# Performance work log

Hardware: AMD Instinct MI355X
Metric: run time of the kernel (lower is better)

Reference implementation:

```python
import jax, jax.numpy as jnp
import numpy as np

NUM_HEADS = 16
TEMPERATURE = 1.0


def setup_inputs() -> dict:
    key = jax.random.key(0)
    ks = jax.random.split(key, 6)
    B, H = 2048, 2048
    return {
        "hidden_states": jax.random.normal(ks[0], (B, H), dtype=jnp.float32),
        "attention_mask": jnp.ones((B,), dtype=bool),
        "Wq": jax.random.normal(ks[1], (H, H), dtype=jnp.float32) * 0.02,
        "Wk": jax.random.normal(ks[2], (H, H), dtype=jnp.float32) * 0.02,
        "Wv": jax.random.normal(ks[3], (H, H), dtype=jnp.float32) * 0.02,
        "Wo": jax.random.normal(ks[4], (H, H), dtype=jnp.float32) * 0.02,
        "scale_param": jnp.full((1,), -3.0, dtype=jnp.float32),
    }


def reference(hidden_states, attention_mask, Wq, Wk, Wv, Wo, scale_param):
    B, H = hidden_states.shape
    nh = NUM_HEADS
    hd = H // nh
    # projections (torch Linear: x @ W.T), reshape to [heads, batch, head_dim]
    q = (hidden_states @ Wq.T).reshape(B, nh, hd).transpose(1, 0, 2)
    k = (hidden_states @ Wk.T).reshape(B, nh, hd).transpose(1, 0, 2)
    v = (hidden_states @ Wv.T).reshape(B, nh, hd).transpose(1, 0, 2)
    # cross-batch scores [heads, B, B]
    scores = jnp.einsum('hqd,hkd->hqk', q, k) / (hd ** 0.5 * TEMPERATURE)
    neg_inf = jnp.float32(-jnp.inf)
    eye = jnp.eye(B, dtype=bool)  # exclude self-attention (diagonal)
    scores = jnp.where(eye[None, :, :], neg_inf, scores)
    scores = jnp.where(attention_mask[None, None, :], scores, neg_inf)
    attn = jax.nn.softmax(scores, axis=-1)
    attn = jnp.nan_to_num(attn, nan=0.0)  # rows fully masked -> 0 (dropout=0 is identity)
    ctx = jnp.einsum('hqk,hkd->hqd', attn, v)  # [heads, B, head_dim]
    ctx = ctx.transpose(1, 0, 2).reshape(B, H)
    cross = ctx @ Wo.T
    scale = jax.nn.sigmoid(scale_param[0])
    return hidden_states + scale * cross
```

## Files before the change

kernel.cpp:

```cpp
#include <hip/hip_runtime.h>

typedef __bf16 bf16;
typedef __attribute__((ext_vector_type(8))) __bf16 bf16x8;
typedef __attribute__((ext_vector_type(4))) float f32x4;
typedef __attribute__((ext_vector_type(4))) short s16x4;

#define HDIM 2048

__device__ __forceinline__ void glds16(const void* g, void* l) {
  __builtin_amdgcn_global_load_lds((const __attribute__((address_space(1))) void*)g,
                                   (__attribute__((address_space(3))) void*)l,
                                   16, 0, 0);
}

#define MFMA16(a, b, c) __builtin_amdgcn_mfma_f32_16x16x32_bf16(a, b, c, 0, 0, 0)

__global__ __launch_bounds__(256) void cvt5(
    const float* __restrict__ s0, const float* __restrict__ s1,
    const float* __restrict__ s2, const float* __restrict__ s3,
    const float* __restrict__ s4,
    bf16* __restrict__ d0, bf16* __restrict__ d1, bf16* __restrict__ d2,
    bf16* __restrict__ d3, bf16* __restrict__ d4) {
  const float* s; bf16* d;
  switch (blockIdx.y) {
    case 0: s = s0; d = d0; break;
    case 1: s = s1; d = d1; break;
    case 2: s = s2; d = d2; break;
    case 3: s = s3; d = d3; break;
    default: s = s4; d = d4; break;
  }
  const size_t base = (size_t)blockIdx.x * 4096 + (threadIdx.x << 2);
  for (int i = 0; i < 4; i++) {
    const float4 v = *(const float4*)(s + base + i * 1024);
    union { bf16 h[4]; s16x4 s4v; } u;
    u.h[0] = (bf16)v.x; u.h[1] = (bf16)v.y; u.h[2] = (bf16)v.z; u.h[3] = (bf16)v.w;
    *(s16x4*)(d + base + i * 1024) = u.s4v;
  }
}

__device__ __forceinline__ void gemm128_core(const bf16* __restrict__ A,
                                             const bf16* __restrict__ B,
                                             int rowBase, int colBase,
                                             f32x4 acc[4][4],
                                             bf16* ldsA, bf16* ldsB) {
  const int t = threadIdx.x;
  const int w = t >> 6, l = t & 63;
  const int wr = (w >> 1) << 6, wc = (w & 1) << 6;
  const int lr = l & 15, lq = l >> 4;

  for (int mi = 0; mi < 4; mi++)
    for (int ni = 0; ni < 4; ni++)
      for (int r = 0; r < 4; r++) acc[mi][ni][r] = 0.f;

  const int sRow = (w << 4) + (l >> 2);
  const int sCol = (l & 3) << 3;
  const bf16* gA = A + (size_t)(rowBase + sRow) * HDIM + sCol;
  const bf16* gB = B + (size_t)(colBase + sRow) * HDIM + sCol;
  bf16* lA = ldsA + (w << 9);
  bf16* lB = ldsB + (w << 9);

  for (int k0 = 0; k0 < HDIM; k0 += 32) {
    glds16(gA, lA);
    glds16(gA + (size_t)64 * HDIM, lA + 2048);
    glds16(gB, lB);
    glds16(gB + (size_t)64 * HDIM, lB + 2048);
    gA += 32; gB += 32;
    __syncthreads();

    bf16x8 af[4], bfr[4];
    for (int mi = 0; mi < 4; mi++)
      af[mi] = *(const bf16x8*)&ldsA[(wr + mi * 16 + lr) * 32 + lq * 8];
    for (int ni = 0; ni < 4; ni++)
      bfr[ni] = *(const bf16x8*)&ldsB[(wc + ni * 16 + lr) * 32 + lq * 8];
    for (int mi = 0; mi < 4; mi++)
      for (int ni = 0; ni < 4; ni++)
        acc[mi][ni] = MFMA16(af[mi], bfr[ni], acc[mi][ni]);
    __syncthreads();
  }
}

__global__ __launch_bounds__(256) void qkv_gemm(
    const bf16* __restrict__ hs, const bf16* __restrict__ Wq,
    const bf16* __restrict__ Wk, const bf16* __restrict__ Wv,
    bf16* __restrict__ qb, bf16* __restrict__ Kf, bf16* __restrict__ Vf) {
  __shared__ bf16 ldsA[128 * 32];
  __shared__ bf16 ldsB[128 * 32];
  const int z = blockIdx.z;
  const bf16* W = (z == 0) ? Wq : (z == 1) ? Wk : Wv;
  const int rowBase = blockIdx.y << 7, colBase = blockIdx.x << 7;
  f32x4 acc[4][4];
  gemm128_core(hs, W, rowBase, colBase, acc, ldsA, ldsB);

  const int t = threadIdx.x;
  const int w = t >> 6, l = t & 63;
  const int wr = (w >> 1) << 6, wc = (w & 1) << 6;
  const int lr = l & 15, lq = l >> 4;

  if (z == 0) {
    for (int mi = 0; mi < 4; mi++)
      for (int ni = 0; ni < 4; ni++) {
        const int col = colBase + wc + ni * 16 + lr;
        const int row0 = rowBase + wr + mi * 16 + lq * 4;
        for (int r = 0; r < 4; r++)
          qb[(size_t)(row0 + r) * HDIM + col] = (bf16)acc[mi][ni][r];
      }
  } else if (z == 1) {
    for (int mi = 0; mi < 4; mi++)
      for (int ni = 0; ni < 4; ni++) {
        const int dim = colBase + wc + ni * 16 + lr;
        const int hh = dim >> 7, ks = (dim >> 5) & 3, kh = (dim >> 3) & 3, j = dim & 7;
        const int row0 = rowBase + wr + mi * 16 + lq * 4;
        for (int r = 0; r < 4; r++) {
          const int key = row0 + r;
          const int kbk = key >> 7, kni = (key >> 4) & 7, kl = key & 15;
          Kf[(((size_t)hh * 16 + kbk) * 32 + kni * 4 + ks) * 512 +
             (kh * 16 + kl) * 8 + j] = (bf16)acc[mi][ni][r];
        }
      }
  } else {
    for (int mi = 0; mi < 4; mi++)
      for (int ni = 0; ni < 4; ni++) {
        const int dim = colBase + wc + ni * 16 + lr;
        const int hh = dim >> 7, vni = (dim >> 4) & 7, ll = dim & 15;
        const int row0 = rowBase + wr + mi * 16 + lq * 4;
        const int kbk = row0 >> 7, ks = (row0 >> 5) & 3, lh = (row0 >> 3) & 3;
        const int j0 = row0 & 7;
        union { bf16 h4[4]; s16x4 v; } u;
        for (int r = 0; r < 4; r++) u.h4[r] = (bf16)acc[mi][ni][r];
        *(s16x4*)&Vf[(((size_t)hh * 16 + kbk) * 32 + vni * 4 + ks) * 512 +
                     (lh * 16 + ll) * 8 + j0] = u.v;
      }
  }
}

__global__ __launch_bounds__(256, 2) void attn_kernel(
    const bf16* __restrict__ qb, const bf16* __restrict__ Kf,
    const bf16* __restrict__ Vf, const unsigned char* __restrict__ amask,
    bf16* __restrict__ ctx) {
  __shared__ bf16 Kl[32 * 512];
  __shared__ bf16 Vl[32 * 512];
  __shared__ bf16 Pl[4 * 16 * 128];

  const int qt = blockIdx.x, h = blockIdx.y;
  const int t = threadIdx.x, w = t >> 6, l = t & 63;
  const int lr = l & 15, lq = l >> 4;
  bf16* Pw = Pl + (w << 11);

  bf16x8 aq[4];
  for (int ks = 0; ks < 4; ks++)
    aq[ks] = *(const bf16x8*)&qb[(size_t)(qt * 64 + w * 16 + lr) * HDIM +
                                 h * 128 + ks * 32 + lq * 8];

  f32x4 o[8];
  for (int ni = 0; ni < 8; ni++)
    for (int r = 0; r < 4; r++) o[ni][r] = 0.f;
  float lsum[4] = {0.f, 0.f, 0.f, 0.f};
  int qrow[4];
  for (int r = 0; r < 4; r++) qrow[r] = qt * 64 + w * 16 + lq * 4 + r;

  const float c = 0.08838834764831845f * 1.4426950408889634f;

  const size_t headOff = (size_t)h * 16 * 32 * 512;
  bf16x8 vtmp[8];
  {
    for (int i = 0; i < 8; i++) {
      const int frag = i * 4 + w;
      glds16(Kf + headOff + frag * 512 + l * 8, Kl + frag * 512);
    }
    for (int i = 0; i < 8; i++) {
      const int frag = i * 4 + w;
      vtmp[i] = *(const bf16x8*)&Vf[headOff + frag * 512 + l * 8];
    }
  }

  for (int kbk = 0; kbk < 16; kbk++) {
    __syncthreads();

    for (int i = 0; i < 8; i++) {
      const int frag = i * 4 + w;
      *(bf16x8*)&Vl[frag * 512 + l * 8] = vtmp[i];
    }

    f32x4 s[8];
    for (int ni = 0; ni < 8; ni++)
      for (int r = 0; r < 4; r++) s[ni][r] = 0.f;
    for (int ks = 0; ks < 4; ks++) {
      bf16x8 bk[8];
      for (int ni = 0; ni < 8; ni++)
        bk[ni] = *(const bf16x8*)&Kl[(ni * 4 + ks) * 512 + l * 8];
      for (int ni = 0; ni < 8; ni++) s[ni] = MFMA16(aq[ks], bk[ni], s[ni]);
    }

    __syncthreads();

    if (kbk < 15) {
      const size_t tileOffN = headOff + (size_t)(kbk + 1) * 32 * 512;
      for (int i = 0; i < 8; i++) {
        const int frag = i * 4 + w;
        glds16(Kf + tileOffN + frag * 512 + l * 8, Kl + frag * 512);
      }
      for (int i = 0; i < 8; i++) {
        const int frag = i * 4 + w;
        vtmp[i] = *(const bf16x8*)&Vf[tileOffN + frag * 512 + l * 8];
      }
    }

    float mk[8];
    for (int ni = 0; ni < 8; ni++)
      mk[ni] = amask[kbk * 128 + ni * 16 + lr] ? 1.f : 0.f;
    const bool diagBlk = (kbk == (qt >> 1));
    for (int ni = 0; ni < 8; ni++) {
      const int col = kbk * 128 + ni * 16 + lr;
      for (int r = 0; r < 4; r++) {
        float p = __builtin_exp2f(s[ni][r] * c) * mk[ni];
        if (diagBlk && col == qrow[r]) p = 0.f;
        s[ni][r] = p;
        lsum[r] += p;
      }
    }

    for (int ni = 0; ni < 8; ni++)
      for (int r = 0; r < 4; r++) {
        const int row = lq * 4 + r;
        Pw[row * 128 + (((ni * 2 + (lr >> 3)) ^ row) << 3) + (lr & 7)] = (bf16)s[ni][r];
      }

    for (int ks = 0; ks < 4; ks++) {
      bf16x8 bv[8];
      for (int ni = 0; ni < 8; ni++)
        bv[ni] = *(const bf16x8*)&Vl[(ni * 4 + ks) * 512 + l * 8];
      const bf16x8 ap = *(const bf16x8*)&Pw[lr * 128 + (((ks * 4 + lq) ^ lr) << 3)];
      for (int ni = 0; ni < 8; ni++) o[ni] = MFMA16(ap, bv[ni], o[ni]);
    }
  }

  for (int r = 0; r < 4; r++)
    for (int off = 1; off < 16; off <<= 1)
      lsum[r] += __shfl_xor(lsum[r], off);

  for (int ni = 0; ni < 8; ni++)
    for (int r = 0; r < 4; r++) {
      const int row = qrow[r];
      const int col = h * 128 + ni * 16 + lr;
      const float li = lsum[r];
      ctx[(size_t)row * HDIM + col] = (bf16)((li > 0.f) ? o[ni][r] / li : 0.f);
    }
}

__global__ __launch_bounds__(256) void out_gemm(
    const bf16* __restrict__ ctx, const bf16* __restrict__ Wo,
    const float* __restrict__ hs, const float* __restrict__ scale_p,
    float* __restrict__ outp) {
  __shared__ bf16 ldsA[128 * 32];
  __shared__ bf16 ldsB[64 * 32];
  const int rowBase = blockIdx.y << 7, colBase = blockIdx.x << 6;
  const int t = threadIdx.x;
  const int w = t >> 6, l = t & 63;
  const int wr = (w >> 1) << 6, wc = (w & 1) << 5;
  const int lr = l & 15, lq = l >> 4;

  f32x4 acc[4][2];
  for (int mi = 0; mi < 4; mi++)
    for (int ni = 0; ni < 2; ni++)
      for (int r = 0; r < 4; r++) acc[mi][ni][r] = 0.f;

  const int sRow = (w << 4) + (l >> 2);
  const int sCol = (l & 3) << 3;
  const bf16* gA = ctx + (size_t)(rowBase + sRow) * HDIM + sCol;
  const bf16* gB = Wo + (size_t)(colBase + sRow) * HDIM + sCol;
  bf16* lA = ldsA + (w << 9);
  bf16* lB = ldsB + (w << 9);

  for (int k0 = 0; k0 < HDIM; k0 += 32) {
    glds16(gA, lA);
    glds16(gA + (size_t)64 * HDIM, lA + 2048);
    glds16(gB, lB);
    gA += 32; gB += 32;
    __syncthreads();

    bf16x8 af[4], bfr[2];
    for (int mi = 0; mi < 4; mi++)
      af[mi] = *(const bf16x8*)&ldsA[(wr + mi * 16 + lr) * 32 + lq * 8];
    for (int ni = 0; ni < 2; ni++)
      bfr[ni] = *(const bf16x8*)&ldsB[(wc + ni * 16 + lr) * 32 + lq * 8];
    for (int mi = 0; mi < 4; mi++)
      for (int ni = 0; ni < 2; ni++)
        acc[mi][ni] = MFMA16(af[mi], bfr[ni], acc[mi][ni]);
    __syncthreads();
  }

  const float sig = 1.0f / (1.0f + __expf(-scale_p[0]));
  for (int mi = 0; mi < 4; mi++)
    for (int ni = 0; ni < 2; ni++) {
      const int col = colBase + wc + ni * 16 + lr;
      const int row0 = rowBase + wr + mi * 16 + lq * 4;
      for (int r = 0; r < 4; r++) {
        const size_t idx = (size_t)(row0 + r) * HDIM + col;
        outp[idx] = hs[idx] + sig * acc[mi][ni][r];
      }
    }
}

extern "C" void kernel_launch(void* const* d_in, const int* in_sizes, int n_in,
                              void* d_out, int out_size, void* d_ws, size_t ws_size,
                              hipStream_t stream) {
  const float* hs = (const float*)d_in[0];
  const unsigned char* amask = (const unsigned char*)d_in[1];
  const float* Wq = (const float*)d_in[2];
  const float* Wk = (const float*)d_in[3];
  const float* Wv = (const float*)d_in[4];
  const float* Wo = (const float*)d_in[5];
  const float* scale_p = (const float*)d_in[6];
  float* outp = (float*)d_out;

  const size_t N = (size_t)HDIM * HDIM;
  bf16* qb   = (bf16*)d_ws;
  bf16* Kf   = qb + N;
  bf16* Vf   = Kf + N;
  bf16* ctx  = Vf + N;
  bf16* hs16 = ctx + N;
  bf16* Wq16 = hs16 + N;
  bf16* Wk16 = Wq16 + N;
  bf16* Wv16 = Wk16 + N;
  bf16* Wo16 = Wv16 + N;

  cvt5<<<dim3(1024, 5), 256, 0, stream>>>(hs, Wq, Wk, Wv, Wo,
                                          hs16, Wq16, Wk16, Wv16, Wo16);
  qkv_gemm<<<dim3(16, 16, 3), 256, 0, stream>>>(hs16, Wq16, Wk16, Wv16, qb, Kf, Vf);
  attn_kernel<<<dim3(32, 16), 256, 0, stream>>>(qb, Kf, Vf, amask, ctx);
  out_gemm<<<dim3(32, 16), 256, 0, stream>>>(ctx, Wo16, hs, scale_p, outp);
}
```

Measured before the change: 278.8 us.

## Double query rows per wave in attention to reuse K/V tiles

Each wave now handles 32 query rows (two 16-row MFMA tiles) instead of 16, so every block covers 128 queries and the grid halves to 16x16 blocks. Each K/V fragment loaded into LDS feeds twice as many MFMAs, which cuts global K/V traffic and LDS reads per unit of work. The mask is folded into the exponent as an additive bias, and the diagonal check runs only on the diagonal block. In exchange the block needs more registers and LDS, occupancy is lowered to one block per SIMD group, and only 256 blocks are launched, which may underfill the device.

Result: slower. 289.0 us (+3.7%).

```diff
diff --git a/kernel.cpp b/kernel.cpp
--- a/kernel.cpp
+++ b/kernel.cpp
@@ -133,44 +133,44 @@
   }
 }
 
-__global__ __launch_bounds__(256, 2) void attn_kernel(
+__global__ __launch_bounds__(256, 1) void attn_kernel(
     const bf16* __restrict__ qb, const bf16* __restrict__ Kf,
     const bf16* __restrict__ Vf, const unsigned char* __restrict__ amask,
     bf16* __restrict__ ctx) {
   __shared__ bf16 Kl[32 * 512];
   __shared__ bf16 Vl[32 * 512];
-  __shared__ bf16 Pl[4 * 16 * 128];
+  __shared__ bf16 Pl[4 * 32 * 128];
 
   const int qt = blockIdx.x, h = blockIdx.y;
   const int t = threadIdx.x, w = t >> 6, l = t & 63;
   const int lr = l & 15, lq = l >> 4;
-  bf16* Pw = Pl + (w << 11);
-
-  bf16x8 aq[4];
-  for (int ks = 0; ks < 4; ks++)
-    aq[ks] = *(const bf16x8*)&qb[(size_t)(qt * 64 + w * 16 + lr) * HDIM +
-                                 h * 128 + ks * 32 + lq * 8];
-
-  f32x4 o[8];
-  for (int ni = 0; ni < 8; ni++)
-    for (int r = 0; r < 4; r++) o[ni][r] = 0.f;
-  float lsum[4] = {0.f, 0.f, 0.f, 0.f};
-  int qrow[4];
-  for (int r = 0; r < 4; r++) qrow[r] = qt * 64 + w * 16 + lq * 4 + r;
+  bf16* Pw = Pl + (w << 12);
+
+  bf16x8 aq[2][4];
+  for (int mi = 0; mi < 2; mi++)
+    for (int ks = 0; ks < 4; ks++)
+      aq[mi][ks] = *(const bf16x8*)&qb[(size_t)(qt * 128 + w * 32 + mi * 16 + lr) * HDIM +
+                                       h * 128 + ks * 32 + lq * 8];
+
+  f32x4 o[2][8];
+  for (int mi = 0; mi < 2; mi++)
+    for (int ni = 0; ni < 8; ni++)
+      for (int r = 0; r < 4; r++) o[mi][ni][r] = 0.f;
+  float lsum[2][4];
+  for (int mi = 0; mi < 2; mi++)
+    for (int r = 0; r < 4; r++) lsum[mi][r] = 0.f;
 
   const float c = 0.08838834764831845f * 1.4426950408889634f;
 
   const size_t headOff = (size_t)h * 16 * 32 * 512;
   bf16x8 vtmp[8];
-  {
-    for (int i = 0; i < 8; i++) {
-      const int frag = i * 4 + w;
-      glds16(Kf + headOff + frag * 512 + l * 8, Kl + frag * 512);
-    }
-    for (int i = 0; i < 8; i++) {
-      const int frag = i * 4 + w;
-      vtmp[i] = *(const bf16x8*)&Vf[headOff + frag * 512 + l * 8];
-    }
+  for (int i = 0; i < 8; i++) {
+    const int frag = i * 4 + w;
+    glds16(Kf + headOff + frag * 512 + l * 8, Kl + frag * 512);
+  }
+  for (int i = 0; i < 8; i++) {
+    const int frag = i * 4 + w;
+    vtmp[i] = *(const bf16x8*)&Vf[headOff + frag * 512 + l * 8];
   }
 
   for (int kbk = 0; kbk < 16; kbk++) {
@@ -181,14 +181,18 @@
       *(bf16x8*)&Vl[frag * 512 + l * 8] = vtmp[i];
     }
 
-    f32x4 s[8];
-    for (int ni = 0; ni < 8; ni++)
-      for (int r = 0; r < 4; r++) s[ni][r] = 0.f;
+    f32x4 s[2][8];
+    for (int mi = 0; mi < 2; mi++)
+      for (int ni = 0; ni < 8; ni++)
+        for (int r = 0; r < 4; r++) s[mi][ni][r] = 0.f;
     for (int ks = 0; ks < 4; ks++) {
       bf16x8 bk[8];
       for (int ni = 0; ni < 8; ni++)
         bk[ni] = *(const bf16x8*)&Kl[(ni * 4 + ks) * 512 + l * 8];
-      for (int ni = 0; ni < 8; ni++) s[ni] = MFMA16(aq[ks], bk[ni], s[ni]);
+      for (int ni = 0; ni < 8; ni++) {
+        s[0][ni] = MFMA16(aq[0][ks], bk[ni], s[0][ni]);
+        s[1][ni] = MFMA16(aq[1][ks], bk[ni], s[1][ni]);
+      }
     }
 
     __syncthreads();
@@ -205,46 +209,65 @@
       }
     }
 
-    float mk[8];
+    float am[8];
     for (int ni = 0; ni < 8; ni++)
-      mk[ni] = amask[kbk * 128 + ni * 16 + lr] ? 1.f : 0.f;
-    const bool diagBlk = (kbk == (qt >> 1));
-    for (int ni = 0; ni < 8; ni++) {
-      const int col = kbk * 128 + ni * 16 + lr;
-      for (int r = 0; r < 4; r++) {
-        float p = __builtin_exp2f(s[ni][r] * c) * mk[ni];
-        if (diagBlk && col == qrow[r]) p = 0.f;
-        s[ni][r] = p;
-        lsum[r] += p;
-      }
-    }
-
-    for (int ni = 0; ni < 8; ni++)
-      for (int r = 0; r < 4; r++) {
-        const int row = lq * 4 + r;
-        Pw[row * 128 + (((ni * 2 + (lr >> 3)) ^ row) << 3) + (lr & 7)] = (bf16)s[ni][r];
-      }
+      am[ni] = amask[kbk * 128 + ni * 16 + lr] ? 0.f : -1e30f;
+    if (kbk == qt) {
+      for (int mi = 0; mi < 2; mi++)
+        for (int ni = 0; ni < 8; ni++) {
+          const int colL = ni * 16 + lr;
+          for (int r = 0; r < 4; r++) {
+            const int rowL = w * 32 + mi * 16 + lq * 4 + r;
+            float p = __builtin_exp2f(s[mi][ni][r] * c + am[ni]);
+            if (colL == rowL) p = 0.f;
+            s[mi][ni][r] = p;
+            lsum[mi][r] += p;
+          }
+        }
+    } else {
+      for (int mi = 0; mi < 2; mi++)
+        for (int ni = 0; ni < 8; ni++)
+          for (int r = 0; r < 4; r++) {
+            const float p = __builtin_exp2f(s[mi][ni][r] * c + am[ni]);
+            s[mi][ni][r] = p;
+            lsum[mi][r] += p;
+          }
+    }
+
+    for (int mi = 0; mi < 2; mi++)
+      for (int ni = 0; ni < 8; ni++)
+        for (int r = 0; r < 4; r++) {
+          const int rl = mi * 16 + lq * 4 + r;
+          Pw[rl * 128 + (((ni * 2 + (lr >> 3)) ^ (lq * 4 + r)) << 3) + (lr & 7)] =
+              (bf16)s[mi][ni][r];
+        }
 
     for (int ks = 0; ks < 4; ks++) {
       bf16x8 bv[8];
       for (int ni = 0; ni < 8; ni++)
         bv[ni] = *(const bf16x8*)&Vl[(ni * 4 + ks) * 512 + l * 8];
-      const bf16x8 ap = *(const bf16x8*)&Pw[lr * 128 + (((ks * 4 + lq) ^ lr) << 3)];
-      for (int ni = 0; ni < 8; ni++) o[ni] = MFMA16(ap, bv[ni], o[ni]);
-    }
-  }
-
-  for (int r = 0; r < 4; r++)
-    for (int off = 1; off < 16; off <<= 1)
-      lsum[r] += __shfl_xor(lsum[r], off);
-
-  for (int ni = 0; ni < 8; ni++)
-    for (int r = 0; r < 4; r++) {
-      const int row = qrow[r];
-      const int col = h * 128 + ni * 16 + lr;
-      const float li = lsum[r];
-      ctx[(size_t)row * HDIM + col] = (bf16)((li > 0.f) ? o[ni][r] / li : 0.f);
-    }
+      const bf16x8 ap0 = *(const bf16x8*)&Pw[lr * 128 + (((ks * 4 + lq) ^ lr) << 3)];
+      const bf16x8 ap1 = *(const bf16x8*)&Pw[(16 + lr) * 128 + (((ks * 4 + lq) ^ lr) << 3)];
+      for (int ni = 0; ni < 8; ni++) {
+        o[0][ni] = MFMA16(ap0, bv[ni], o[0][ni]);
+        o[1][ni] = MFMA16(ap1, bv[ni], o[1][ni]);
+      }
+    }
+  }
+
+  for (int mi = 0; mi < 2; mi++)
+    for (int r = 0; r < 4; r++)
+      for (int off = 1; off < 16; off <<= 1)
+        lsum[mi][r] += __shfl_xor(lsum[mi][r], off);
+
+  for (int mi = 0; mi < 2; mi++)
+    for (int ni = 0; ni < 8; ni++)
+      for (int r = 0; r < 4; r++) {
+        const int row = qt * 128 + w * 32 + mi * 16 + lq * 4 + r;
+        const int col = h * 128 + ni * 16 + lr;
+        const float li = lsum[mi][r];
+        ctx[(size_t)row * HDIM + col] = (bf16)((li > 0.f) ? o[mi][ni][r] / li : 0.f);
+      }
 }
 
 __global__ __launch_bounds__(256) void out_gemm(
@@ -327,6 +350,6 @@
   cvt5<<<dim3(1024, 5), 256, 0, stream>>>(hs, Wq, Wk, Wv, Wo,
                                           hs16, Wq16, Wk16, Wv16, Wo16);
   qkv_gemm<<<dim3(16, 16, 3), 256, 0, stream>>>(hs16, Wq16, Wk16, Wv16, qb, Kf, Vf);
-  attn_kernel<<<dim3(32, 16), 256, 0, stream>>>(qb, Kf, Vf, amask, ctx);
+  attn_kernel<<<dim3(16, 16), 256, 0, stream>>>(qb, Kf, Vf, amask, ctx);
   out_gemm<<<dim3(32, 16), 256, 0, stream>>>(ctx, Wo16, hs, scale_p, outp);
 }
```
